# Performance work log

Hardware: AMD Instinct MI355X
Metric: run time of the kernel (lower is better)

Reference implementation:

```python
import jax, jax.numpy as jnp
import numpy as np

N = 50000      # nodes
E = 800000     # edges (avg degree 16)
S = 2          # sample_size
D_IN = 128     # input_dim
D_NOISE = 64   # noise_dim
D0 = 256       # output_dims[0]
D1 = 256       # output_dims[1]


def setup_inputs() -> dict:
    key = jax.random.key(0)
    ks = jax.random.split(key, 8)
    X = jax.random.normal(ks[0], (1, N, D_IN), dtype=jnp.float32)
    edge_src = jax.random.randint(ks[1], (E,), 0, N)
    edge_dst = jax.random.randint(ks[2], (E,), 0, N)
    # Bernoulli(0.5) noise, as in torch.distributions.Bernoulli
    epsilon = (jax.random.uniform(ks[3], (S, N, D_NOISE)) < 0.5).astype(jnp.float32)
    W0 = jax.random.normal(ks[4], (D_IN + D_NOISE, D0), dtype=jnp.float32) * 0.05
    b0 = jnp.zeros((D0,), jnp.float32)
    W1 = jax.random.normal(ks[5], (D0, D1), dtype=jnp.float32) * 0.05
    b1 = jnp.zeros((D1,), jnp.float32)
    eps0 = jnp.zeros((), jnp.float32)  # GINConv learnable eps, init 0
    eps1 = jnp.zeros((), jnp.float32)
    return dict(X=X, epsilon=epsilon, edge_src=edge_src, edge_dst=edge_dst,
                W0=W0, b0=b0, W1=W1, b1=b1, eps0=eps0, eps1=eps1)


def reference(X, epsilon, edge_src, edge_dst, W0, b0, W1, b1, eps0, eps1):
    # Expand features over sample dim and concat noise: [S, N, D_IN + D_NOISE]
    feat = jnp.broadcast_to(X, (epsilon.shape[0], X.shape[1], X.shape[2]))
    h = jnp.concatenate([feat, epsilon], axis=2)

    def gin_layer(h, eps, W, b):
        # sum aggregation over in-edges: agg[:, d] += h[:, s] for each edge (s, d)
        agg = jnp.zeros_like(h).at[:, edge_dst, :].add(h[:, edge_src, :])
        return jax.nn.relu(((1.0 + eps) * h + agg) @ W + b)

    h = gin_layer(h, eps0, W0, b0)
    h = gin_layer(h, eps1, W1, b1)
    out = jax.nn.relu(h)  # outer activation applied once more in forward()
    return out, epsilon
```

## Files before the change

### kernel.cpp

```cpp
#include <hip/hip_runtime.h>
#include <hip/hip_bf16.h>

#define NN 50000
#define NE 800000
#define NS 2
#define DIN 128
#define DNOISE 64
#define DH0 192
#define DOUT 256
#define NB 49

typedef __bf16 bf16x8 __attribute__((ext_vector_type(8)));
typedef float floatx4 __attribute__((ext_vector_type(4)));


__device__ inline float bflo(unsigned int u) { return __uint_as_float(u << 16); }
__device__ inline float bfhi(unsigned int u) { return __uint_as_float(u & 0xffff0000u); }
__device__ inline unsigned short f2bf_bits(float x) {
    __hip_bfloat16 b = __float2bfloat16(x);
    return *reinterpret_cast<unsigned short*>(&b);
}
__device__ inline unsigned int pack2(float lo, float hi) {
    return (unsigned int)f2bf_bits(lo) | ((unsigned int)f2bf_bits(hi) << 16);
}


__global__ void count_kernel(const int* __restrict__ dst, int* __restrict__ cnt) {
    int i = blockIdx.x * blockDim.x + threadIdx.x;
    if (i < NE) atomicAdd(&cnt[dst[i]], 1);
}

__global__ __launch_bounds__(1024) void scanA_kernel(const int* __restrict__ cnt, int* __restrict__ bsum) {
    int i = blockIdx.x * 1024 + threadIdx.x;
    int v = (i < NN) ? cnt[i] : 0;
    for (int off = 32; off > 0; off >>= 1) v += __shfl_down(v, off);
    __shared__ int wsum[16];
    if ((threadIdx.x & 63) == 0) wsum[threadIdx.x >> 6] = v;
    __syncthreads();
    if (threadIdx.x == 0) {
        int s = 0;
        for (int k = 0; k < 16; ++k) s += wsum[k];
        bsum[blockIdx.x] = s;
    }
}

__global__ __launch_bounds__(64) void scanB_kernel(int* __restrict__ bsum) {
    int lane = threadIdx.x;
    int orig = (lane < NB) ? bsum[lane] : 0;
    int v = orig;
    for (int off = 1; off < 64; off <<= 1) {
        int t = __shfl_up(v, off);
        if (lane >= off) v += t;
    }
    if (lane < NB) bsum[lane] = v - orig;
}

__global__ __launch_bounds__(1024) void scanC_kernel(int* __restrict__ cnt, const int* __restrict__ bsum,
                                                     int* __restrict__ row_ptr) {
    __shared__ int buf[1024];
    int tid = threadIdx.x;
    int i = blockIdx.x * 1024 + tid;
    int v = (i < NN) ? cnt[i] : 0;
    buf[tid] = v;
    __syncthreads();
    for (int off = 1; off < 1024; off <<= 1) {
        int t = (tid >= off) ? buf[tid - off] : 0;
        __syncthreads();
        buf[tid] += t;
        __syncthreads();
    }
    int excl = buf[tid] - v + bsum[blockIdx.x];
    if (i < NN) { row_ptr[i + 1] = excl + v; cnt[i] = excl; }
    if (i == 0) row_ptr[0] = 0;
}

__global__ void fill_kernel(const int* __restrict__ src, const int* __restrict__ dst,
                            int* __restrict__ cursor, int* __restrict__ col_idx) {
    int i = blockIdx.x * blockDim.x + threadIdx.x;
    if (i < NE) {
        int p = atomicAdd(&cursor[dst[i]], 1);
        col_idx[p] = src[i];
    }
}

#define XQ (NN * DIN / 4)
#define XB4 ((XQ + 255) / 256)
#define NR_BLOCKS ((NS * NN + 255) / 256)

__global__ void prep_kernel(const float* __restrict__ X, unsigned short* __restrict__ Xb,
                            const float* __restrict__ noise, uint2* __restrict__ Nbit,
                            float* __restrict__ out_eps) {
    int b = blockIdx.x;
    if (b < XB4) {
        int i = b * 256 + threadIdx.x;
        if (i < XQ) {
            float4 v = reinterpret_cast<const float4*>(X)[i];
            ushort4 o;
            o.x = f2bf_bits(v.x); o.y = f2bf_bits(v.y); o.z = f2bf_bits(v.z); o.w = f2bf_bits(v.w);
            reinterpret_cast<ushort4*>(Xb)[i] = o;
        }
    } else {
        int r = (b - XB4) * 256 + threadIdx.x;
        if (r < NS * NN) {
            const float4* p = reinterpret_cast<const float4*>(noise + (size_t)r * DNOISE);
            float4* oe = reinterpret_cast<float4*>(out_eps + (size_t)r * DNOISE);
            unsigned int lo = 0, hi = 0;
            for (int q = 0; q < 8; ++q) {
                float4 v = p[q];
                oe[q] = v;
                int base = q * 4;
                lo |= (v.x != 0.f ? 1u : 0u) << base;
                lo |= (v.y != 0.f ? 1u : 0u) << (base + 1);
                lo |= (v.z != 0.f ? 1u : 0u) << (base + 2);
                lo |= (v.w != 0.f ? 1u : 0u) << (base + 3);
            }
            for (int q = 8; q < 16; ++q) {
                float4 v = p[q];
                oe[q] = v;
                int base = q * 4 - 32;
                hi |= (v.x != 0.f ? 1u : 0u) << base;
                hi |= (v.y != 0.f ? 1u : 0u) << (base + 1);
                hi |= (v.z != 0.f ? 1u : 0u) << (base + 2);
                hi |= (v.w != 0.f ? 1u : 0u) << (base + 3);
            }
            uint2 o; o.x = lo; o.y = hi;
            Nbit[r] = o;
        }
    }
}


template <int K>
__global__ void pack_w(const float* __restrict__ W, uint4* __restrict__ Wp) {
    const int n = blockIdx.x;
    const int tj = threadIdx.x;
    if (tj < K / 8) {
        unsigned short h[8];
#pragma unroll
        for (int r = 0; r < 8; ++r)
            h[r] = f2bf_bits(W[(size_t)(tj * 8 + r) * DOUT + n]);
        uint4 o;
        o.x = (unsigned)h[0] | ((unsigned)h[1] << 16);
        o.y = (unsigned)h[2] | ((unsigned)h[3] << 16);
        o.z = (unsigned)h[4] | ((unsigned)h[5] << 16);
        o.w = (unsigned)h[6] | ((unsigned)h[7] << 16);
        Wp[(size_t)((n >> 6) * (K / 8) + tj) * 64 + (n & 63)] = o;
    }
}


__global__ __launch_bounds__(256) void agg0_kernel(
    const unsigned int* __restrict__ Xb,
    const uint2* __restrict__ Nbit,
    const int* __restrict__ row_ptr, const int* __restrict__ col_idx,
    const float* __restrict__ eps0p,
    unsigned int* __restrict__ z0) {
    const int d = blockIdx.x * 2 + (threadIdx.x >> 7);
    const int cc = threadIdx.x & 127;
    const float c = 1.f + eps0p[0];
    const int beg = row_ptr[d], end = row_ptr[d + 1];
    if (cc < 64) {
        const unsigned int* src = Xb + cc;
        unsigned int u = src[(size_t)d * 64];
        float aL = c * bflo(u), aH = c * bfhi(u);
        int e = beg;
        for (; e + 3 < end; e += 4) {
            int i0 = col_idx[e], i1 = col_idx[e + 1], i2 = col_idx[e + 2], i3 = col_idx[e + 3];
            unsigned int u0 = src[(size_t)i0 * 64], u1 = src[(size_t)i1 * 64];
            unsigned int u2 = src[(size_t)i2 * 64], u3 = src[(size_t)i3 * 64];
            aL += (bflo(u0) + bflo(u1)) + (bflo(u2) + bflo(u3));
            aH += (bfhi(u0) + bfhi(u1)) + (bfhi(u2) + bfhi(u3));
        }
        for (; e < end; ++e) {
            unsigned int ue = src[(size_t)col_idx[e] * 64];
            aL += bflo(ue); aH += bfhi(ue);
        }
        unsigned int r = pack2(aL, aH);
        z0[(size_t)d * 96 + cc] = r;
        z0[(size_t)(NN + d) * 96 + cc] = r;
    } else {
        int j = cc - 64;
        int s = j >> 5, col = j & 31;
        const uint2* src = Nbit + (size_t)s * NN;
        const int word = col >> 4;
        const int sh = (2 * col) & 31;
        uint2 uS = src[d];
        unsigned int wS = word ? uS.y : uS.x;
        int c0 = 0, c1 = 0;
        int e = beg;
        for (; e + 3 < end; e += 4) {
            uint2 u0 = src[col_idx[e]], u1 = src[col_idx[e + 1]];
            uint2 u2 = src[col_idx[e + 2]], u3 = src[col_idx[e + 3]];
            unsigned int w0 = word ? u0.y : u0.x, w1 = word ? u1.y : u1.x;
            unsigned int w2 = word ? u2.y : u2.x, w3 = word ? u3.y : u3.x;
            c0 += (int)((w0 >> sh) & 1) + (int)((w1 >> sh) & 1) + (int)((w2 >> sh) & 1) + (int)((w3 >> sh) & 1);
            c1 += (int)((w0 >> (sh + 1)) & 1) + (int)((w1 >> (sh + 1)) & 1) +
                  (int)((w2 >> (sh + 1)) & 1) + (int)((w3 >> (sh + 1)) & 1);
        }
        for (; e < end; ++e) {
            uint2 ue = src[col_idx[e]];
            unsigned int we = word ? ue.y : ue.x;
            c0 += (int)((we >> sh) & 1);
            c1 += (int)((we >> (sh + 1)) & 1);
        }
        float aL = c * (float)((wS >> sh) & 1) + (float)c0;
        float aH = c * (float)((wS >> (sh + 1)) & 1) + (float)c1;
        z0[(size_t)(s * NN + d) * 96 + 64 + col] = pack2(aL, aH);
    }
}


__global__ __launch_bounds__(256) void agg1_kernel(
    const uint2* __restrict__ h,
    const int* __restrict__ row_ptr, const int* __restrict__ col_idx,
    const float* __restrict__ eps1p,
    uint2* __restrict__ z1) {
    const int d = blockIdx.x * 2 + (threadIdx.x >> 7);
    const int s = (threadIdx.x >> 6) & 1;
    const int cc = threadIdx.x & 63;
    const float c = 1.f + eps1p[0];
    const int beg = row_ptr[d], end = row_ptr[d + 1];
    const uint2* src = h + (size_t)s * NN * 64 + cc;
    uint2 u = src[(size_t)d * 64];
    float aL0 = c * bflo(u.x), aH0 = c * bfhi(u.x);
    float aL1 = c * bflo(u.y), aH1 = c * bfhi(u.y);
    int e = beg;
    for (; e + 7 < end; e += 8) {
        uint2 g[8];
#pragma unroll
        for (int q = 0; q < 8; ++q) g[q] = src[(size_t)col_idx[e + q] * 64];
#pragma unroll
        for (int q = 0; q < 8; ++q) {
            aL0 += bflo(g[q].x); aH0 += bfhi(g[q].x);
            aL1 += bflo(g[q].y); aH1 += bfhi(g[q].y);
        }
    }
    for (; e + 3 < end; e += 4) {
        uint2 u0 = src[(size_t)col_idx[e] * 64], u1 = src[(size_t)col_idx[e + 1] * 64];
        uint2 u2 = src[(size_t)col_idx[e + 2] * 64], u3 = src[(size_t)col_idx[e + 3] * 64];
        aL0 += (bflo(u0.x) + bflo(u1.x)) + (bflo(u2.x) + bflo(u3.x));
        aH0 += (bfhi(u0.x) + bfhi(u1.x)) + (bfhi(u2.x) + bfhi(u3.x));
        aL1 += (bflo(u0.y) + bflo(u1.y)) + (bflo(u2.y) + bflo(u3.y));
        aH1 += (bfhi(u0.y) + bfhi(u1.y)) + (bfhi(u2.y) + bfhi(u3.y));
    }
    for (; e < end; ++e) {
        uint2 ue = src[(size_t)col_idx[e] * 64];
        aL0 += bflo(ue.x); aH0 += bfhi(ue.x);
        aL1 += bflo(ue.y); aH1 += bfhi(ue.y);
    }
    uint2 r; r.x = pack2(aL0, aH0); r.y = pack2(aL1, aH1);
    z1[(size_t)(s * NN + d) * 64 + cc] = r;
}


template <bool NT>
__device__ inline void st_out(float* C, size_t idx, float v) {
    if (NT) __builtin_nontemporal_store(v, C + idx); else C[idx] = v;
}
template <bool NT>
__device__ inline void st_out(__hip_bfloat16* C, size_t idx, float v) { C[idx] = __float2bfloat16(v); }

#define GEMM_GRID 3128

template <int K, bool NT, typename OUT_T>
__global__ __launch_bounds__(256, 4) void gemm_bias_relu(
    const __hip_bfloat16* __restrict__ A, const uint4* __restrict__ Wp,
    const float* __restrict__ bias, OUT_T* __restrict__ C, int M) {
    constexpr int NJ = K / 8;
    __shared__ uint4 lds[NJ * 64];

    const int p = blockIdx.x;
    const int l = (p & 7) * (GEMM_GRID / 8) + (p >> 3);
    const int cg = l & 3;
    const int rg = l >> 2;
    const int blockRow = rg * 128;

    const int tid = threadIdx.x;
    const uint4* wsrc = Wp + (size_t)cg * (NJ * 64);
#pragma unroll
    for (int i = 0; i < NJ / 4; ++i)
        lds[i * 256 + tid] = wsrc[i * 256 + tid];
    __syncthreads();

    const int lane = tid & 63, wave = tid >> 6;
    const int lo = lane & 15, quad = lane >> 4;
    const int rowBase = blockRow + wave * 32;

    floatx4 acc[2][4];
#pragma unroll
    for (int i = 0; i < 2; ++i)
#pragma unroll
        for (int j = 0; j < 4; ++j) acc[i][j] = (floatx4){0.f, 0.f, 0.f, 0.f};

    unsigned int aoff[2];
#pragma unroll
    for (int rt = 0; rt < 2; ++rt) {
        int rowi = rowBase + rt * 16 + lo;
        if (rowi >= M) rowi = M - 1;
        aoff[rt] = (unsigned int)rowi * (unsigned int)(K * 2);
    }
    const char* Ab = (const char*)A + quad * 16;

#pragma unroll
    for (int ks = 0; ks < K / 32; ++ks) {
        bf16x8 a[2], b[4];
#pragma unroll
        for (int rt = 0; rt < 2; ++rt)
            a[rt] = *(const bf16x8*)(Ab + aoff[rt] + ks * 64);
#pragma unroll
        for (int ct = 0; ct < 4; ++ct)
            b[ct] = *(const bf16x8*)&lds[(ks * 4 + quad) * 64 + ct * 16 + lo];
#pragma unroll
        for (int rt = 0; rt < 2; ++rt)
#pragma unroll
            for (int ct = 0; ct < 4; ++ct)
                acc[rt][ct] = __builtin_amdgcn_mfma_f32_16x16x32_bf16(a[rt], b[ct], acc[rt][ct], 0, 0, 0);
    }

#pragma unroll
    for (int ct = 0; ct < 4; ++ct) {
        const int col = cg * 64 + ct * 16 + lo;
        const float bv = bias[col];
#pragma unroll
        for (int rt = 0; rt < 2; ++rt) {
#pragma unroll
            for (int r = 0; r < 4; ++r) {
                int row = rowBase + rt * 16 + quad * 4 + r;
                if (row < M) {
                    float v = acc[rt][ct][r] + bv;
                    st_out<NT>(C, (size_t)row * DOUT + col, v > 0.f ? v : 0.f);
                }
            }
        }
    }
}

extern "C" void kernel_launch(void* const* d_in, const int* in_sizes, int n_in,
                              void* d_out, int out_size, void* d_ws, size_t ws_size,
                              hipStream_t stream) {
    const float* X = (const float*)d_in[0];
    const float* noise = (const float*)d_in[1];
    const int* esrc = (const int*)d_in[2];
    const int* edst = (const int*)d_in[3];
    const float* W0 = (const float*)d_in[4];
    const float* b0 = (const float*)d_in[5];
    const float* W1 = (const float*)d_in[6];
    const float* b1 = (const float*)d_in[7];
    const float* eps0 = (const float*)d_in[8];
    const float* eps1 = (const float*)d_in[9];
    float* out = (float*)d_out;

    const int M = NS * NN;

    char* w = (char*)d_ws;
    auto carve = [&](size_t bytes) { char* p = w; w += (bytes + 511) & ~(size_t)511; return p; };
    int* cursor = (int*)carve((size_t)NN * 4);
    int* row_ptr = (int*)carve((size_t)(NN + 1) * 4);
    int* col_idx = (int*)carve((size_t)NE * 4);
    int* bsum = (int*)carve((size_t)NB * 4);
    uint2* Nbit = (uint2*)carve((size_t)M * 8);
    uint4* Wp0 = (uint4*)carve((size_t)DH0 * DOUT * 2);
    uint4* Wp1 = (uint4*)carve((size_t)DOUT * DOUT * 2);
    unsigned int* z = (unsigned int*)carve((size_t)M * DOUT * 2);

    __hip_bfloat16* h1 = (__hip_bfloat16*)d_out;
    unsigned short* Xb = (unsigned short*)(z + (size_t)M * 96);

    hipMemsetAsync(cursor, 0, (size_t)NN * 4, stream);
    count_kernel<<<(NE + 255) / 256, 256, 0, stream>>>(edst, cursor);
    scanA_kernel<<<NB, 1024, 0, stream>>>(cursor, bsum);
    scanB_kernel<<<1, 64, 0, stream>>>(bsum);
    scanC_kernel<<<NB, 1024, 0, stream>>>(cursor, bsum, row_ptr);
    fill_kernel<<<(NE + 255) / 256, 256, 0, stream>>>(esrc, edst, cursor, col_idx);
    prep_kernel<<<XB4 + NR_BLOCKS, 256, 0, stream>>>(X, Xb, noise, Nbit,
                                                     out + (size_t)M * DOUT);
    pack_w<DH0><<<DOUT, 64, 0, stream>>>(W0, Wp0);
    pack_w<DOUT><<<DOUT, 64, 0, stream>>>(W1, Wp1);

    agg0_kernel<<<NN / 2, 256, 0, stream>>>(
        (const unsigned int*)Xb, Nbit, row_ptr, col_idx, eps0, z);
    gemm_bias_relu<DH0, false, __hip_bfloat16><<<GEMM_GRID, 256, 0, stream>>>(
        (const __hip_bfloat16*)z, Wp0, b0, h1, M);
    agg1_kernel<<<NN / 2, 256, 0, stream>>>(
        (const uint2*)h1, row_ptr, col_idx, eps1, (uint2*)z);
    gemm_bias_relu<DOUT, true, float><<<GEMM_GRID, 256, 0, stream>>>(
        (const __hip_bfloat16*)z, Wp1, b1, out, M);
}
```

Before: 595.7 us.

## Fuse layer-0 aggregation with GEMM via swizzled shared-memory tile

Merges the layer-0 neighbor aggregation and the bias+ReLU GEMM into one kernel. Each block aggregates 32 nodes for both samples into a swizzled LDS tile of 64 rows by 192 bf16 values, then runs MFMA directly from LDS against the packed weights. This removes the global write and re-read of the intermediate z buffer and one kernel launch. It also unrolls the feature gather to 8 edges. The trade-off is fewer and larger blocks: each block now handles 16 serial aggregation iterations, and the GEMM tiles shrink to 64 rows, so weights are re-read per block with less reuse.

```diff
diff --git a/kernel.cpp b/kernel.cpp
--- a/kernel.cpp
+++ b/kernel.cpp
@@ -149,65 +149,131 @@
 }
 
 
-__global__ __launch_bounds__(256) void agg0_kernel(
+__global__ __launch_bounds__(256, 4) void fused0_kernel(
     const unsigned int* __restrict__ Xb,
     const uint2* __restrict__ Nbit,
     const int* __restrict__ row_ptr, const int* __restrict__ col_idx,
     const float* __restrict__ eps0p,
-    unsigned int* __restrict__ z0) {
-    const int d = blockIdx.x * 2 + (threadIdx.x >> 7);
-    const int cc = threadIdx.x & 127;
+    const uint4* __restrict__ Wp,
+    const float* __restrict__ bias,
+    __hip_bfloat16* __restrict__ H) {
+    __shared__ unsigned int zt[64 * 96];
+    const int n0 = blockIdx.x * 32;
+    const int tid = threadIdx.x;
     const float c = 1.f + eps0p[0];
-    const int beg = row_ptr[d], end = row_ptr[d + 1];
-    if (cc < 64) {
-        const unsigned int* src = Xb + cc;
-        unsigned int u = src[(size_t)d * 64];
-        float aL = c * bflo(u), aH = c * bfhi(u);
-        int e = beg;
-        for (; e + 3 < end; e += 4) {
-            int i0 = col_idx[e], i1 = col_idx[e + 1], i2 = col_idx[e + 2], i3 = col_idx[e + 3];
-            unsigned int u0 = src[(size_t)i0 * 64], u1 = src[(size_t)i1 * 64];
-            unsigned int u2 = src[(size_t)i2 * 64], u3 = src[(size_t)i3 * 64];
-            aL += (bflo(u0) + bflo(u1)) + (bflo(u2) + bflo(u3));
-            aH += (bfhi(u0) + bfhi(u1)) + (bfhi(u2) + bfhi(u3));
-        }
-        for (; e < end; ++e) {
-            unsigned int ue = src[(size_t)col_idx[e] * 64];
-            aL += bflo(ue); aH += bfhi(ue);
-        }
-        unsigned int r = pack2(aL, aH);
-        z0[(size_t)d * 96 + cc] = r;
-        z0[(size_t)(NN + d) * 96 + cc] = r;
-    } else {
-        int j = cc - 64;
-        int s = j >> 5, col = j & 31;
-        const uint2* src = Nbit + (size_t)s * NN;
-        const int word = col >> 4;
-        const int sh = (2 * col) & 31;
-        uint2 uS = src[d];
-        unsigned int wS = word ? uS.y : uS.x;
-        int c0 = 0, c1 = 0;
-        int e = beg;
-        for (; e + 3 < end; e += 4) {
-            uint2 u0 = src[col_idx[e]], u1 = src[col_idx[e + 1]];
-            uint2 u2 = src[col_idx[e + 2]], u3 = src[col_idx[e + 3]];
-            unsigned int w0 = word ? u0.y : u0.x, w1 = word ? u1.y : u1.x;
-            unsigned int w2 = word ? u2.y : u2.x, w3 = word ? u3.y : u3.x;
-            c0 += (int)((w0 >> sh) & 1) + (int)((w1 >> sh) & 1) + (int)((w2 >> sh) & 1) + (int)((w3 >> sh) & 1);
-            c1 += (int)((w0 >> (sh + 1)) & 1) + (int)((w1 >> (sh + 1)) & 1) +
-                  (int)((w2 >> (sh + 1)) & 1) + (int)((w3 >> (sh + 1)) & 1);
-        }
-        for (; e < end; ++e) {
-            uint2 ue = src[col_idx[e]];
-            unsigned int we = word ? ue.y : ue.x;
-            c0 += (int)((we >> sh) & 1);
-            c1 += (int)((we >> (sh + 1)) & 1);
-        }
-        float aL = c * (float)((wS >> sh) & 1) + (float)c0;
-        float aH = c * (float)((wS >> (sh + 1)) & 1) + (float)c1;
-        z0[(size_t)(s * NN + d) * 96 + 64 + col] = pack2(aL, aH);
-    }
-}
+
+    for (int jj = 0; jj < 16; ++jj) {
+        const int d = n0 + jj * 2 + (tid >> 7);
+        if (d < NN) {
+            const int nloc = d - n0;
+            const int cc = tid & 127;
+            const int beg = row_ptr[d], end = row_ptr[d + 1];
+            if (cc < 64) {
+                const unsigned int* src = Xb + cc;
+                unsigned int u = src[(size_t)d * 64];
+                float aL = c * bflo(u), aH = c * bfhi(u);
+                int e = beg;
+                for (; e + 7 < end; e += 8) {
+                    unsigned int g0 = src[(size_t)col_idx[e] * 64];
+                    unsigned int g1 = src[(size_t)col_idx[e + 1] * 64];
+                    unsigned int g2 = src[(size_t)col_idx[e + 2] * 64];
+                    unsigned int g3 = src[(size_t)col_idx[e + 3] * 64];
+                    unsigned int g4 = src[(size_t)col_idx[e + 4] * 64];
+                    unsigned int g5 = src[(size_t)col_idx[e + 5] * 64];
+                    unsigned int g6 = src[(size_t)col_idx[e + 6] * 64];
+                    unsigned int g7 = src[(size_t)col_idx[e + 7] * 64];
+                    aL += (bflo(g0) + bflo(g1)) + (bflo(g2) + bflo(g3));
+                    aH += (bfhi(g0) + bfhi(g1)) + (bfhi(g2) + bfhi(g3));
+                    aL += (bflo(g4) + bflo(g5)) + (bflo(g6) + bflo(g7));
+                    aH += (bfhi(g4) + bfhi(g5)) + (bfhi(g6) + bfhi(g7));
+                }
+                for (; e + 3 < end; e += 4) {
+                    unsigned int g0 = src[(size_t)col_idx[e] * 64];
+                    unsigned int g1 = src[(size_t)col_idx[e + 1] * 64];
+                    unsigned int g2 = src[(size_t)col_idx[e + 2] * 64];
+                    unsigned int g3 = src[(size_t)col_idx[e + 3] * 64];
+                    aL += (bflo(g0) + bflo(g1)) + (bflo(g2) + bflo(g3));
+                    aH += (bfhi(g0) + bfhi(g1)) + (bfhi(g2) + bfhi(g3));
+                }
+                for (; e < end; ++e) {
+                    unsigned int ue = src[(size_t)col_idx[e] * 64];
+                    aL += bflo(ue); aH += bfhi(ue);
+                }
+                unsigned int r = pack2(aL, aH);
+                const int r1 = 32 + nloc;
+                zt[(nloc * 96 + cc) ^ ((nloc & 7) << 2)] = r;
+                zt[(r1 * 96 + cc) ^ ((r1 & 7) << 2)] = r;
+            } else {
+                int j = cc - 64;
+                int s = j >> 5, col = j & 31;
+                const uint2* src = Nbit + (size_t)s * NN;
+                const int word = col >> 4;
+                const int sh = (2 * col) & 31;
+                uint2 uS = src[d];
+                unsigned int wS = word ? uS.y : uS.x;
+                int c0 = 0, c1 = 0;
+                int e = beg;
+                for (; e + 3 < end; e += 4) {
+                    uint2 u0 = src[col_idx[e]], u1 = src[col_idx[e + 1]];
+                    uint2 u2 = src[col_idx[e + 2]], u3 = src[col_idx[e + 3]];
+                    unsigned int w0 = word ? u0.y : u0.x, w1 = word ? u1.y : u1.x;
+                    unsigned int w2 = word ? u2.y : u2.x, w3 = word ? u3.y : u3.x;
+                    c0 += (int)((w0 >> sh) & 1) + (int)((w1 >> sh) & 1) + (int)((w2 >> sh) & 1) + (int)((w3 >> sh) & 1);
+                    c1 += (int)((w0 >> (sh + 1)) & 1) + (int)((w1 >> (sh + 1)) & 1) +
+                          (int)((w2 >> (sh + 1)) & 1) + (int)((w3 >> (sh + 1)) & 1);
+                }
+                for (; e < end; ++e) {
+                    uint2 ue = src[col_idx[e]];
+                    unsigned int we = word ? ue.y : ue.x;
+                    c0 += (int)((we >> sh) & 1);
+                    c1 += (int)((we >> (sh + 1)) & 1);
+                }
+                float aL = c * (float)((wS >> sh) & 1) + (float)c0;
+                float aH = c * (float)((wS >> (sh + 1)) & 1) + (float)c1;
+                const int lr = s * 32 + nloc;
+                zt[(lr * 96 + 64 + col) ^ ((lr & 7) << 2)] = pack2(aL, aH);
+            }
+        }
+    }
+    __syncthreads();
+
+    const int lane = tid & 63, w = tid >> 6;
+    const int lo = lane & 15, quad = lane >> 4;
+    const int lrow = w * 16 + lo;
+
+    floatx4 acc[16];
+#pragma unroll
+    for (int t = 0; t < 16; ++t) acc[t] = (floatx4){0.f, 0.f, 0.f, 0.f};
+
+    const uint4* zt4 = (const uint4*)zt;
+    for (int ks = 0; ks < 6; ++ks) {
+        bf16x8 a = *(const bf16x8*)&zt4[(lrow * 24 + ks * 4 + quad) ^ (lrow & 7)];
+#pragma unroll
+        for (int ct = 0; ct < 16; ++ct) {
+            bf16x8 b = *(const bf16x8*)&Wp[(size_t)((ct >> 2) * 24 + ks * 4 + quad) * 64 + (ct & 3) * 16 + lo];
+            acc[ct] = __builtin_amdgcn_mfma_f32_16x16x32_bf16(a, b, acc[ct], 0, 0, 0);
+        }
+    }
+
+    const int mbase = w * 16 + quad * 4;
+#pragma unroll
+    for (int ct = 0; ct < 16; ++ct) {
+        const int col = (ct >> 2) * 64 + (ct & 3) * 16 + lo;
+        const float bv = bias[col];
+#pragma unroll
+        for (int r = 0; r < 4; ++r) {
+            const int m = mbase + r;
+            const int node = n0 + (m & 31);
+            if (node < NN) {
+                const int grow = (m >> 5) * NN + node;
+                float v = acc[ct][r] + bv;
+                H[(size_t)grow * DOUT + col] = __float2bfloat16(v > 0.f ? v : 0.f);
+            }
+        }
+    }
+}
+
+#define FUSED0_GRID ((NN + 31) / 32)
 
 
 __global__ __launch_bounds__(256) void agg1_kernel(
@@ -377,10 +443,8 @@
     pack_w<DH0><<<DOUT, 64, 0, stream>>>(W0, Wp0);
     pack_w<DOUT><<<DOUT, 64, 0, stream>>>(W1, Wp1);
 
-    agg0_kernel<<<NN / 2, 256, 0, stream>>>(
-        (const unsigned int*)Xb, Nbit, row_ptr, col_idx, eps0, z);
-    gemm_bias_relu<DH0, false, __hip_bfloat16><<<GEMM_GRID, 256, 0, stream>>>(
-        (const __hip_bfloat16*)z, Wp0, b0, h1, M);
+    fused0_kernel<<<FUSED0_GRID, 256, 0, stream>>>(
+        (const unsigned int*)Xb, Nbit, row_ptr, col_idx, eps0, Wp0, b0, h1);
     agg1_kernel<<<NN / 2, 256, 0, stream>>>(
         (const uint2*)h1, row_ptr, col_idx, eps1, (uint2*)z);
     gemm_bias_relu<DOUT, true, float><<<GEMM_GRID, 256, 0, stream>>>(
```

Measured after the change: 624.1 us. +4.8%, slower.

## Fuse layer-1 aggregation with GEMM via shared-memory tile

Applied to the files above, without the earlier changes.

Replaces the separate layer-1 gather kernel and GEMM kernel with one fused kernel. Each block aggregates 16 nodes across both samples into a swizzled LDS tile, then runs MFMA against the packed W1 and writes the ReLU output directly. This removes the global round-trip of the aggregated bf16 intermediate and one launch. The cost is that W1 is re-read from global/L2 by every block with no LDS staging, occupancy may be lower, and the workspace buffers are remapped so the layer-0 intermediate lives in the output buffer.

```diff
diff --git a/kernel.cpp b/kernel.cpp
--- a/kernel.cpp
+++ b/kernel.cpp
@@ -210,49 +210,6 @@
 }
 
 
-__global__ __launch_bounds__(256) void agg1_kernel(
-    const uint2* __restrict__ h,
-    const int* __restrict__ row_ptr, const int* __restrict__ col_idx,
-    const float* __restrict__ eps1p,
-    uint2* __restrict__ z1) {
-    const int d = blockIdx.x * 2 + (threadIdx.x >> 7);
-    const int s = (threadIdx.x >> 6) & 1;
-    const int cc = threadIdx.x & 63;
-    const float c = 1.f + eps1p[0];
-    const int beg = row_ptr[d], end = row_ptr[d + 1];
-    const uint2* src = h + (size_t)s * NN * 64 + cc;
-    uint2 u = src[(size_t)d * 64];
-    float aL0 = c * bflo(u.x), aH0 = c * bfhi(u.x);
-    float aL1 = c * bflo(u.y), aH1 = c * bfhi(u.y);
-    int e = beg;
-    for (; e + 7 < end; e += 8) {
-        uint2 g[8];
-#pragma unroll
-        for (int q = 0; q < 8; ++q) g[q] = src[(size_t)col_idx[e + q] * 64];
-#pragma unroll
-        for (int q = 0; q < 8; ++q) {
-            aL0 += bflo(g[q].x); aH0 += bfhi(g[q].x);
-            aL1 += bflo(g[q].y); aH1 += bfhi(g[q].y);
-        }
-    }
-    for (; e + 3 < end; e += 4) {
-        uint2 u0 = src[(size_t)col_idx[e] * 64], u1 = src[(size_t)col_idx[e + 1] * 64];
-        uint2 u2 = src[(size_t)col_idx[e + 2] * 64], u3 = src[(size_t)col_idx[e + 3] * 64];
-        aL0 += (bflo(u0.x) + bflo(u1.x)) + (bflo(u2.x) + bflo(u3.x));
-        aH0 += (bfhi(u0.x) + bfhi(u1.x)) + (bfhi(u2.x) + bfhi(u3.x));
-        aL1 += (bflo(u0.y) + bflo(u1.y)) + (bflo(u2.y) + bflo(u3.y));
-        aH1 += (bfhi(u0.y) + bfhi(u1.y)) + (bfhi(u2.y) + bfhi(u3.y));
-    }
-    for (; e < end; ++e) {
-        uint2 ue = src[(size_t)col_idx[e] * 64];
-        aL0 += bflo(ue.x); aH0 += bfhi(ue.x);
-        aL1 += bflo(ue.y); aH1 += bfhi(ue.y);
-    }
-    uint2 r; r.x = pack2(aL0, aH0); r.y = pack2(aL1, aH1);
-    z1[(size_t)(s * NN + d) * 64 + cc] = r;
-}
-
-
 template <bool NT>
 __device__ inline void st_out(float* C, size_t idx, float v) {
     if (NT) __builtin_nontemporal_store(v, C + idx); else C[idx] = v;
@@ -334,6 +291,95 @@
         }
     }
 }
+
+
+__global__ __launch_bounds__(256, 6) void fused1_kernel(
+    const uint2* __restrict__ h,
+    const int* __restrict__ row_ptr, const int* __restrict__ col_idx,
+    const float* __restrict__ eps1p,
+    const uint4* __restrict__ Wp,
+    const float* __restrict__ bias,
+    float* __restrict__ out) {
+    __shared__ uint2 zt[32 * 64];
+    const int n0 = blockIdx.x * 16;
+    const int tid = threadIdx.x;
+    const float c = 1.f + eps1p[0];
+
+    for (int jj = 0; jj < 8; ++jj) {
+        const int d = n0 + jj * 2 + (tid >> 7);
+        const int nloc = d - n0;
+        const int s = (tid >> 6) & 1;
+        const int cc = tid & 63;
+        const int beg = row_ptr[d], end = row_ptr[d + 1];
+        const uint2* src = h + (size_t)s * NN * 64 + cc;
+        uint2 u = src[(size_t)d * 64];
+        float aL0 = c * bflo(u.x), aH0 = c * bfhi(u.x);
+        float aL1 = c * bflo(u.y), aH1 = c * bfhi(u.y);
+        int e = beg;
+        for (; e + 7 < end; e += 8) {
+            uint2 g[8];
+#pragma unroll
+            for (int q = 0; q < 8; ++q) g[q] = src[(size_t)col_idx[e + q] * 64];
+#pragma unroll
+            for (int q = 0; q < 8; ++q) {
+                aL0 += bflo(g[q].x); aH0 += bfhi(g[q].x);
+                aL1 += bflo(g[q].y); aH1 += bfhi(g[q].y);
+            }
+        }
+        for (; e + 3 < end; e += 4) {
+            uint2 u0 = src[(size_t)col_idx[e] * 64], u1 = src[(size_t)col_idx[e + 1] * 64];
+            uint2 u2 = src[(size_t)col_idx[e + 2] * 64], u3 = src[(size_t)col_idx[e + 3] * 64];
+            aL0 += (bflo(u0.x) + bflo(u1.x)) + (bflo(u2.x) + bflo(u3.x));
+            aH0 += (bfhi(u0.x) + bfhi(u1.x)) + (bfhi(u2.x) + bfhi(u3.x));
+            aL1 += (bflo(u0.y) + bflo(u1.y)) + (bflo(u2.y) + bflo(u3.y));
+            aH1 += (bfhi(u0.y) + bfhi(u1.y)) + (bfhi(u2.y) + bfhi(u3.y));
+        }
+        for (; e < end; ++e) {
+            uint2 ue = src[(size_t)col_idx[e] * 64];
+            aL0 += bflo(ue.x); aH0 += bfhi(ue.x);
+            aL1 += bflo(ue.y); aH1 += bfhi(ue.y);
+        }
+        uint2 r; r.x = pack2(aL0, aH0); r.y = pack2(aL1, aH1);
+        const int lr = s * 16 + nloc;
+        zt[lr * 64 + (((cc >> 1) ^ (lr & 7)) << 1) + (cc & 1)] = r;
+    }
+    __syncthreads();
+
+    const int lane = tid & 63, w = tid >> 6;
+    const int lo = lane & 15, quad = lane >> 4;
+    const int rw = w >> 1, ch = w & 1;
+    const int lrow = rw * 16 + lo;
+
+    floatx4 acc[8];
+#pragma unroll
+    for (int t = 0; t < 8; ++t) acc[t] = (floatx4){0.f, 0.f, 0.f, 0.f};
+
+    const uint4* zt4 = (const uint4*)zt;
+#pragma unroll
+    for (int ks = 0; ks < 8; ++ks) {
+        bf16x8 a = *(const bf16x8*)&zt4[lrow * 32 + ((ks * 4 + quad) ^ (lrow & 7))];
+#pragma unroll
+        for (int ct = 0; ct < 8; ++ct) {
+            bf16x8 b = *(const bf16x8*)&Wp[(size_t)((ch * 2 + (ct >> 2)) * 32 + ks * 4 + quad) * 64 + (ct & 3) * 16 + lo];
+            acc[ct] = __builtin_amdgcn_mfma_f32_16x16x32_bf16(a, b, acc[ct], 0, 0, 0);
+        }
+    }
+
+#pragma unroll
+    for (int ct = 0; ct < 8; ++ct) {
+        const int col = ch * 128 + ct * 16 + lo;
+        const float bv = bias[col];
+#pragma unroll
+        for (int r = 0; r < 4; ++r) {
+            const int mrow = rw * 16 + quad * 4 + r;
+            const int grow = (mrow >> 4) * NN + n0 + (mrow & 15);
+            float v = acc[ct][r] + bv;
+            __builtin_nontemporal_store(v > 0.f ? v : 0.f, out + (size_t)grow * DOUT + col);
+        }
+    }
+}
+
+#define FUSED1_GRID (NN / 16)
 
 extern "C" void kernel_launch(void* const* d_in, const int* in_sizes, int n_in,
                               void* d_out, int out_size, void* d_ws, size_t ws_size,
@@ -361,10 +407,11 @@
     uint2* Nbit = (uint2*)carve((size_t)M * 8);
     uint4* Wp0 = (uint4*)carve((size_t)DH0 * DOUT * 2);
     uint4* Wp1 = (uint4*)carve((size_t)DOUT * DOUT * 2);
-    unsigned int* z = (unsigned int*)carve((size_t)M * DOUT * 2);
-
-    __hip_bfloat16* h1 = (__hip_bfloat16*)d_out;
-    unsigned short* Xb = (unsigned short*)(z + (size_t)M * 96);
+    char* zreg = carve((size_t)M * DOUT * 2);
+
+    unsigned int* z0 = (unsigned int*)d_out;
+    unsigned short* Xb = (unsigned short*)(zreg + (size_t)M * 96 * 4);
+    __hip_bfloat16* h1 = (__hip_bfloat16*)zreg;
 
     hipMemsetAsync(cursor, 0, (size_t)NN * 4, stream);
     count_kernel<<<(NE + 255) / 256, 256, 0, stream>>>(edst, cursor);
@@ -378,11 +425,9 @@
     pack_w<DOUT><<<DOUT, 64, 0, stream>>>(W1, Wp1);
 
     agg0_kernel<<<NN / 2, 256, 0, stream>>>(
-        (const unsigned int*)Xb, Nbit, row_ptr, col_idx, eps0, z);
+        (const unsigned int*)Xb, Nbit, row_ptr, col_idx, eps0, z0);
     gemm_bias_relu<DH0, false, __hip_bfloat16><<<GEMM_GRID, 256, 0, stream>>>(
-        (const __hip_bfloat16*)z, Wp0, b0, h1, M);
-    agg1_kernel<<<NN / 2, 256, 0, stream>>>(
-        (const uint2*)h1, row_ptr, col_idx, eps1, (uint2*)z);
-    gemm_bias_relu<DOUT, true, float><<<GEMM_GRID, 256, 0, stream>>>(
-        (const __hip_bfloat16*)z, Wp1, b1, out, M);
-}
+        (const __hip_bfloat16*)z0, Wp0, b0, h1, M);
+    fused1_kernel<<<FUSED1_GRID, 256, 0, stream>>>(
+        (const uint2*)h1, row_ptr, col_idx, eps1, Wp1, b1, out);
+}
```

Result: faster. 571.4 us (-4.1%).
